# Performance work log

Measured on AMD Instinct MI355X. Metric: run time of the kernel, lower is better.

## Reference

```python
import jax, jax.numpy as jnp
import numpy as np

B, S, D, H = 2, 2048, 2048, 16
HD = D // H
ALIBI_BIAS_MAX = 8
NEG_INF = -1e9  # used only via float('-inf') literal below


def build_attn_mask(n_heads, seq_len, alibi_bias_max=8, dtype=jnp.float32):
    # causal mask: -inf strictly above diagonal
    causal = jnp.triu(jnp.full((seq_len, seq_len), -jnp.inf, dtype=dtype), k=1)
    # full alibi bias: -|i-j| scaled per head by 1/2**(m_h)
    rel = jnp.arange(1 - seq_len, 1, dtype=dtype)  # [S]
    bias = rel[None, :] - rel[:, None]             # [S,S]
    bias = -jnp.abs(bias)
    m = jnp.arange(1, n_heads + 1, dtype=dtype) * (alibi_bias_max / n_heads)
    slopes = 1.0 / (2.0 ** m)                      # [H]
    a_bias = bias[None, :, :] * slopes[:, None, None]  # [H,S,S]
    return causal[None, :, :] + a_bias


def setup_inputs() -> dict:
    key = jax.random.key(0)
    ks = jax.random.split(key, 6)
    x = jax.random.normal(ks[0], (B, S, D), dtype=jnp.float32)
    key_padding_mask = jnp.ones((B, S), dtype=bool)  # True = keep (module inverts before torch)
    attn_mask = build_attn_mask(H, S, ALIBI_BIAS_MAX)
    scale = 1.0 / np.sqrt(D)
    in_proj_w = jax.random.normal(ks[1], (3 * D, D), dtype=jnp.float32) * scale
    in_proj_b = jax.random.normal(ks[2], (3 * D,), dtype=jnp.float32) * 0.01
    out_w = jax.random.normal(ks[3], (D, D), dtype=jnp.float32) * scale
    out_b = jax.random.normal(ks[4], (D,), dtype=jnp.float32) * 0.01
    return {"x": x, "key_padding_mask": key_padding_mask, "attn_mask": attn_mask,
            "in_proj_w": in_proj_w, "in_proj_b": in_proj_b,
            "out_w": out_w, "out_b": out_b}


def reference(x, key_padding_mask, attn_mask, in_proj_w, in_proj_b, out_w, out_b):
    # fused QKV projection (torch MultiheadAttention in_proj)
    qkv = jnp.einsum('bsd,ed->bse', x, in_proj_w) + in_proj_b  # [B,S,3D]
    q, k, v = jnp.split(qkv, 3, axis=-1)
    # [B,H,S,hd]
    q = q.reshape(B, S, H, HD).transpose(0, 2, 1, 3)
    k = k.reshape(B, S, H, HD).transpose(0, 2, 1, 3)
    v = v.reshape(B, S, H, HD).transpose(0, 2, 1, 3)
    scores = jnp.einsum('bhqd,bhkd->bhqk', q, k) / jnp.sqrt(jnp.float32(HD))
    scores = scores + attn_mask[None]  # causal + alibi, [1,H,S,S]
    # key_padding_mask True = keep; masked keys -> -inf
    scores = jnp.where(key_padding_mask[:, None, None, :], scores, -jnp.inf)
    attn = jax.nn.softmax(scores, axis=-1)  # [B,H,S,S]
    ctx = jnp.einsum('bhqk,bhkd->bhqd', attn, v)
    ctx = ctx.transpose(0, 2, 1, 3).reshape(B, S, D)
    out = jnp.einsum('bsd,ed->bse', ctx, out_w) + out_b
    # need_weights=True, average_attn_weights default True -> mean over heads
    avg_attn = attn.mean(axis=1)  # [B,S,S]
    return out, avg_attn
```

## Files before the change

kernel.cpp:

```cpp
#include <hip/hip_runtime.h>
#include <math.h>

#define BB 2
#define SS 2048
#define DD 2048
#define HH 16
#define HDIM 128
#define QKVP 6144
#define NEG_INIT  -1.0e30f
#define NEG_CLAMP -3.0e4f

typedef __attribute__((ext_vector_type(8))) short s8v;
typedef __attribute__((ext_vector_type(4))) float f4v;

__device__ __forceinline__ short f2bf(float f) {
  unsigned u = __float_as_uint(f);
  unsigned r = (u + 0x7FFFu + ((u >> 16) & 1u)) >> 16;
  return (short)(unsigned short)r;
}

__global__ void conv_bf16(const float* __restrict__ src, short* __restrict__ dst,
                          int n8) {
  int t = blockIdx.x * blockDim.x + threadIdx.x;
  if (t >= n8) return;
  const float* s = src + (size_t)t * 8;
  s8v o;
#pragma unroll
  for (int i = 0; i < 8; i++) o[i] = f2bf(s[i]);
  ((s8v*)dst)[t] = o;
}

template <typename TOUT>
__global__ __launch_bounds__(256) void gemm_bt_bias(
    const short* __restrict__ A, const short* __restrict__ Bm,
    const float* __restrict__ bias, TOUT* __restrict__ C,
    int M, int N, int K)
{
  __shared__ short As[128 * 72];
  __shared__ short Bs[128 * 72];
  const int tid = threadIdx.x;
  const int lane = tid & 63, wid = tid >> 6;
  const int wm = wid >> 1, wn = wid & 1;
  const int ln = lane & 15, quad = lane >> 4;
  const int m0 = blockIdx.y * 128, n0 = blockIdx.x * 128;

  f4v acc[4][4];
#pragma unroll
  for (int i = 0; i < 4; i++)
#pragma unroll
    for (int j = 0; j < 4; j++) acc[i][j] = {0.f, 0.f, 0.f, 0.f};

  const int row = tid >> 1;
  const int ch  = (tid & 1) * 32;

  const s8v* ag = (const s8v*)(A + (size_t)(m0 + row) * K + ch);
  const s8v* bg = (const s8v*)(Bm + (size_t)(n0 + row) * K + ch);
  s8v a0 = ag[0], a1 = ag[1], a2 = ag[2], a3 = ag[3];
  s8v b0 = bg[0], b1 = bg[1], b2 = bg[2], b3 = bg[3];

  for (int kt = 0; kt < K; kt += 64) {
    __syncthreads();
    *(s8v*)&As[row * 72 + ch +  0] = a0;
    *(s8v*)&As[row * 72 + ch +  8] = a1;
    *(s8v*)&As[row * 72 + ch + 16] = a2;
    *(s8v*)&As[row * 72 + ch + 24] = a3;
    *(s8v*)&Bs[row * 72 + ch +  0] = b0;
    *(s8v*)&Bs[row * 72 + ch +  8] = b1;
    *(s8v*)&Bs[row * 72 + ch + 16] = b2;
    *(s8v*)&Bs[row * 72 + ch + 24] = b3;
    if (kt + 64 < K) {
      const s8v* an = (const s8v*)(A + (size_t)(m0 + row) * K + kt + 64 + ch);
      const s8v* bn = (const s8v*)(Bm + (size_t)(n0 + row) * K + kt + 64 + ch);
      a0 = an[0]; a1 = an[1]; a2 = an[2]; a3 = an[3];
      b0 = bn[0]; b1 = bn[1]; b2 = bn[2]; b3 = bn[3];
    }
    __syncthreads();
#pragma unroll
    for (int kc = 0; kc < 2; kc++) {
      s8v af[4], bfr[4];
#pragma unroll
      for (int i = 0; i < 4; i++)
        af[i] = *(const s8v*)&As[(wm * 64 + i * 16 + ln) * 72 + kc * 32 + quad * 8];
#pragma unroll
      for (int j = 0; j < 4; j++)
        bfr[j] = *(const s8v*)&Bs[(wn * 64 + j * 16 + ln) * 72 + kc * 32 + quad * 8];
#pragma unroll
      for (int i = 0; i < 4; i++)
#pragma unroll
        for (int j = 0; j < 4; j++)
          acc[i][j] = __builtin_amdgcn_mfma_f32_16x16x32_bf16(af[i], bfr[j], acc[i][j], 0, 0, 0);
    }
  }
#pragma unroll
  for (int j = 0; j < 4; j++) {
    int col = n0 + wn * 64 + j * 16 + ln;
    float bv = bias[col];
#pragma unroll
    for (int i = 0; i < 4; i++) {
      int rbase = m0 + wm * 64 + i * 16 + quad * 4;
#pragma unroll
      for (int r = 0; r < 4; r++) {
        float val = acc[i][j][r] + bv;
        if constexpr (sizeof(TOUT) == 4)
          C[(size_t)(rbase + r) * N + col] = val;
        else
          C[(size_t)(rbase + r) * N + col] = f2bf(val);
      }
    }
  }
}

__global__ __launch_bounds__(256) void transpose_v(const short* __restrict__ qkv,
                                                   short* __restrict__ vT) {
  __shared__ short tile[64 * 72];
  const int bh = blockIdx.z;
  const int b = bh >> 4;
  const int hsel = bh & 15;
  const int s0 = blockIdx.x * 64;
  const int hd0 = blockIdx.y * 64;
  const int t = threadIdx.x;
  const int r = t >> 3, c8 = t & 7;
#pragma unroll
  for (int half = 0; half < 2; half++) {
    int rr = r + half * 32;
    s8v v = *(const s8v*)&qkv[(size_t)(b * SS + s0 + rr) * QKVP + 4096 + hsel * HDIM + hd0 + c8 * 8];
    *(s8v*)&tile[rr * 72 + c8 * 8] = v;
  }
  __syncthreads();
#pragma unroll
  for (int half = 0; half < 2; half++) {
    int rr = r + half * 32;
    s8v o;
#pragma unroll
    for (int j = 0; j < 8; j++) o[j] = tile[(c8 * 8 + j) * 72 + rr];
    *(s8v*)&vT[((size_t)bh * HDIM + hd0 + rr) * SS + s0 + c8 * 8] = o;
  }
}

__global__ __launch_bounds__(512, 4) void flash_fwd(
    const short* __restrict__ qkv, const short* __restrict__ vT,
    float* __restrict__ lse, short* __restrict__ ctx)
{
  __shared__ short Ks[64 * 136];
  __shared__ short Vs[128 * 72];
  __shared__ short plds[8][16 * 72];

  const int g = blockIdx.x;
  const int b = g >> 8;
  const int h = (g >> 4) & 15;
  const int qh = g & 15;
  const int qt = b ? qh : 15 - qh;

  const int bh = b * HH + h;
  const int tid = threadIdx.x, lane = tid & 63, wid = tid >> 6;
  const int ln = lane & 15, quad = lane >> 4;
  const int q0 = qt * 128 + wid * 16;

  const short* qb = qkv + (size_t)b * SS * QKVP + h * HDIM;
  const short* kb = qb + 2048;
  const short* vb = vT + (size_t)bh * HDIM * SS;

  const int krow = tid >> 3, kc0 = (tid & 7) * 8;
  const int vrow = tid >> 2, vc0 = (tid & 3) * 8;
  const short* kgp = kb + (size_t)krow * QKVP + kc0;
  const short* vgp = vb + (size_t)vrow * SS + vc0;
  short* kls = &Ks[krow * 136 + kc0];
  short* vls = &Vs[vrow * 72 + vc0];

  const float slope = exp2f(-0.5f * (float)(h + 1));
  const float scale = 0.08838834764831845f;

  s8v aq[4];
#pragma unroll
  for (int kc = 0; kc < 4; kc++)
    aq[kc] = *(const s8v*)&qb[(size_t)(q0 + ln) * QKVP + kc * 32 + quad * 8];

  s8v k0r = ((const s8v*)kgp)[0], k1r = *(const s8v*)(kgp + 64);
  s8v v0r = ((const s8v*)vgp)[0], v1r = *(const s8v*)(vgp + 32);

  f4v o[8];
#pragma unroll
  for (int d = 0; d < 8; d++) o[d] = {0.f, 0.f, 0.f, 0.f};
  float mrow[4], lrow[4];
#pragma unroll
  for (int r = 0; r < 4; r++) { mrow[r] = NEG_INIT; lrow[r] = 0.0f; }

  const int nkt = 2 * qt + 2;
  for (int kt = 0; kt < nkt; kt++) {
    __syncthreads();
    *(s8v*)kls = k0r;  *(s8v*)(kls + 64) = k1r;
    *(s8v*)vls = v0r;  *(s8v*)(vls + 32) = v1r;
    if (kt < nkt - 1) {
      const short* kn = kgp + (size_t)(kt + 1) * 64 * QKVP;
      const short* vn = vgp + (kt + 1) * 64;
      k0r = ((const s8v*)kn)[0]; k1r = *(const s8v*)(kn + 64);
      v0r = ((const s8v*)vn)[0]; v1r = *(const s8v*)(vn + 32);
    }
    __syncthreads();

    if (kt * 64 > q0 + 15) continue;

    f4v sacc[4];
#pragma unroll
    for (int ks = 0; ks < 4; ks++) {
      f4v z = {0.f, 0.f, 0.f, 0.f};
#pragma unroll
      for (int kc = 0; kc < 4; kc++) {
        s8v bk = *(const s8v*)&Ks[(ks * 16 + ln) * 136 + kc * 32 + quad * 8];
        z = __builtin_amdgcn_mfma_f32_16x16x32_bf16(aq[kc], bk, z, 0, 0, 0);
      }
      sacc[ks] = z;
    }
    float sv[4][4];
#pragma unroll
    for (int ks = 0; ks < 4; ks++)
#pragma unroll
      for (int r = 0; r < 4; r++) {
        int i = q0 + quad * 4 + r;
        int j = kt * 64 + ks * 16 + ln;
        int di = i - j;
        sv[ks][r] = (di >= 0) ? fmaf(sacc[ks][r], scale, -(float)di * slope)
                              : NEG_CLAMP;
      }
    float mnew[4], al[4];
#pragma unroll
    for (int r = 0; r < 4; r++) {
      float mx = fmaxf(fmaxf(sv[0][r], sv[1][r]), fmaxf(sv[2][r], sv[3][r]));
#pragma unroll
      for (int off = 1; off < 16; off <<= 1)
        mx = fmaxf(mx, __shfl_xor(mx, off, 64));
      mnew[r] = fmaxf(mrow[r], mx);
      al[r] = __expf(mrow[r] - mnew[r]);
      mrow[r] = mnew[r];
    }
    float ps[4] = {0.f, 0.f, 0.f, 0.f};
    short pb[4][4];
#pragma unroll
    for (int ks = 0; ks < 4; ks++)
#pragma unroll
      for (int r = 0; r < 4; r++) {
        float p = __expf(sv[ks][r] - mnew[r]);
        ps[r] += p;
        pb[ks][r] = f2bf(p);
      }
#pragma unroll
    for (int r = 0; r < 4; r++) {
      float s = ps[r];
#pragma unroll
      for (int off = 1; off < 16; off <<= 1) s += __shfl_xor(s, off, 64);
      lrow[r] = lrow[r] * al[r] + s;
    }
#pragma unroll
    for (int d = 0; d < 8; d++)
#pragma unroll
      for (int r = 0; r < 4; r++) o[d][r] *= al[r];
#pragma unroll
    for (int ks = 0; ks < 4; ks++)
#pragma unroll
      for (int r = 0; r < 4; r++)
        plds[wid][(quad * 4 + r) * 72 + ks * 16 + ln] = pb[ks][r];
#pragma unroll
    for (int kc2 = 0; kc2 < 2; kc2++) {
      s8v ap = *(const s8v*)&plds[wid][ln * 72 + kc2 * 32 + quad * 8];
#pragma unroll
      for (int d = 0; d < 8; d++) {
        s8v bv = *(const s8v*)&Vs[(d * 16 + ln) * 72 + kc2 * 32 + quad * 8];
        o[d] = __builtin_amdgcn_mfma_f32_16x16x32_bf16(ap, bv, o[d], 0, 0, 0);
      }
    }
  }
  float inv[4];
#pragma unroll
  for (int r = 0; r < 4; r++) inv[r] = 1.0f / lrow[r];
#pragma unroll
  for (int d = 0; d < 8; d++)
#pragma unroll
    for (int r = 0; r < 4; r++) {
      int qrow = q0 + quad * 4 + r;
      ctx[((size_t)(b * SS + qrow)) * DD + h * HDIM + d * 16 + ln] = f2bf(o[d][r] * inv[r]);
    }
#pragma unroll
  for (int r = 0; r < 4; r++)
    if (ln == r)
      lse[(size_t)bh * SS + q0 + quad * 4 + r] = mrow[r] + __logf(lrow[r]);
}

__global__ __launch_bounds__(512, 4) void avg_attn_kernel(
    const short* __restrict__ qkv, const float* __restrict__ lse,
    float* __restrict__ avg)
{
  __shared__ short Ks[64 * 136];
  const int ktile = blockIdx.x, qtile = blockIdx.y, b = blockIdx.z;
  const int tid = threadIdx.x, lane = tid & 63, wid = tid >> 6;
  const int ln = lane & 15, quad = lane >> 4;
  const int q0 = qtile * 128 + wid * 16;
  const int k0 = ktile * 64;
  float acc[4][4];
#pragma unroll
  for (int ks = 0; ks < 4; ks++)
#pragma unroll
    for (int r = 0; r < 4; r++) acc[ks][r] = 0.0f;

  if (ktile <= 2 * qtile + 1) {
    const float scale = 0.08838834764831845f;
    const int krow = tid >> 3, kc0 = (tid & 7) * 8;
    const short* kg0 = qkv + (size_t)(b * SS + k0 + krow) * QKVP + 2048 + kc0;
    short* kls = &Ks[krow * 136 + kc0];
    s8v k0r = ((const s8v*)kg0)[0], k1r = *(const s8v*)(kg0 + 64);
    const bool wactive = (k0 <= q0 + 15);
    for (int hh = 0; hh < HH; hh++) {
      __syncthreads();
      *(s8v*)kls = k0r;  *(s8v*)(kls + 64) = k1r;
      if (hh < HH - 1) {
        const short* kn = kg0 + (hh + 1) * HDIM;
        k0r = ((const s8v*)kn)[0]; k1r = *(const s8v*)(kn + 64);
      }
      __syncthreads();
      if (wactive) {
        const int bh = b * HH + hh;
        const float slope = exp2f(-0.5f * (float)(hh + 1));
        const short* qb = qkv + (size_t)b * SS * QKVP + hh * HDIM;
        s8v aq[4];
#pragma unroll
        for (int kc = 0; kc < 4; kc++)
          aq[kc] = *(const s8v*)&qb[(size_t)(q0 + ln) * QKVP + kc * 32 + quad * 8];
        float lsev[4];
#pragma unroll
        for (int r = 0; r < 4; r++) lsev[r] = lse[(size_t)bh * SS + q0 + quad * 4 + r];
#pragma unroll
        for (int ks = 0; ks < 4; ks++) {
          f4v z = {0.f, 0.f, 0.f, 0.f};
#pragma unroll
          for (int kc = 0; kc < 4; kc++) {
            s8v bk = *(const s8v*)&Ks[(ks * 16 + ln) * 136 + kc * 32 + quad * 8];
            z = __builtin_amdgcn_mfma_f32_16x16x32_bf16(aq[kc], bk, z, 0, 0, 0);
          }
#pragma unroll
          for (int r = 0; r < 4; r++) {
            int i = q0 + quad * 4 + r;
            int j = k0 + ks * 16 + ln;
            int di = i - j;
            float svv = (di >= 0) ? fmaf(z[r], scale, -(float)di * slope) : NEG_CLAMP;
            acc[ks][r] += __expf(svv - lsev[r]);
          }
        }
      }
    }
  }
  const float inv16 = 1.0f / 16.0f;
#pragma unroll
  for (int ks = 0; ks < 4; ks++)
#pragma unroll
    for (int r = 0; r < 4; r++)
      avg[((size_t)b * SS + q0 + quad * 4 + r) * SS + k0 + ks * 16 + ln] =
          acc[ks][r] * inv16;
}

extern "C" void kernel_launch(void* const* d_in, const int* in_sizes, int n_in,
                              void* d_out, int out_size, void* d_ws, size_t ws_size,
                              hipStream_t stream)
{
  const float *x = nullptr, *w_in = nullptr, *b_in = nullptr,
              *w_out = nullptr, *b_out = nullptr;
  for (int idx = 0; idx < n_in; idx++) {
    switch (in_sizes[idx]) {
      case 8388608:  x     = (const float*)d_in[idx]; break;
      case 12582912: w_in  = (const float*)d_in[idx]; break;
      case 6144:     b_in  = (const float*)d_in[idx]; break;
      case 4194304:  w_out = (const float*)d_in[idx]; break;
      case 2048:     b_out = (const float*)d_in[idx]; break;
      default: break;
    }
  }

  char* ws = (char*)d_ws;
  short* qkv = (short*)(ws);
  short* xb  = (short*)(ws + 50331648);
  short* vT  = (short*)(ws + 50331648);
  short* wib = (short*)(ws + 67108864);
  short* ctx = (short*)(ws + 67108864);
  float* lse = (float*)(ws + 83886080);
  short* wob = (short*)(ws + 92274688);

  float* outp = (float*)d_out;
  float* avgp = outp + (size_t)BB * SS * DD;

  conv_bf16<<<4096, 256, 0, stream>>>(x, xb, 1048576);
  conv_bf16<<<6144, 256, 0, stream>>>(w_in, wib, 1572864);
  conv_bf16<<<2048, 256, 0, stream>>>(w_out, wob, 524288);

  gemm_bt_bias<short><<<dim3(QKVP / 128, (BB * SS) / 128), 256, 0, stream>>>(
      xb, wib, b_in, qkv, BB * SS, QKVP, DD);
  transpose_v<<<dim3(32, 2, 32), 256, 0, stream>>>(qkv, vT);
  flash_fwd<<<dim3(512, 1, 1), 512, 0, stream>>>(qkv, vT, lse, ctx);
  avg_attn_kernel<<<dim3(32, 16, 2), 512, 0, stream>>>(qkv, lse, avgp);
  gemm_bt_bias<float><<<dim3(DD / 128, (BB * SS) / 128), 256, 0, stream>>>(
      ctx, wob, b_out, outp, BB * SS, DD, DD);
}
```

Baseline: 719.9 us.

## Use direct global-to-LDS loads in GEMM, widen avg-attn key tiles, skip masked subtiles

The GEMM now stages A/B tiles with global_load_lds (direct-to-LDS) instead of a register double buffer, and drops the LDS row padding. This removes VGPR staging and store instructions but also loses the prefetch overlap and padding, so LDS bank conflicts are possible. The avg-attention kernel processes 128-key tiles per block, halving redundant Q/LSE reloads, and skips fully masked 16-key subtiles per wave. Flash forward also skips the QK MFMAs for masked 16-key subtiles on diagonal tiles.

```diff
diff --git a/kernel.cpp b/kernel.cpp
--- a/kernel.cpp
+++ b/kernel.cpp
@@ -13,6 +13,13 @@
 typedef __attribute__((ext_vector_type(8))) short s8v;
 typedef __attribute__((ext_vector_type(4))) float f4v;
 
+typedef const unsigned __attribute__((address_space(1)))* gas_ptr;
+typedef unsigned __attribute__((address_space(3)))* las_ptr;
+
+__device__ __forceinline__ void gld16(const short* g, short* l) {
+  __builtin_amdgcn_global_load_lds((gas_ptr)g, (las_ptr)l, 16, 0, 0);
+}
+
 __device__ __forceinline__ short f2bf(float f) {
   unsigned u = __float_as_uint(f);
   unsigned r = (u + 0x7FFFu + ((u >> 16) & 1u)) >> 16;
@@ -36,8 +43,8 @@
     const float* __restrict__ bias, TOUT* __restrict__ C,
     int M, int N, int K)
 {
-  __shared__ short As[128 * 72];
-  __shared__ short Bs[128 * 72];
+  __shared__ short As[128 * 64];
+  __shared__ short Bs[128 * 64];
   const int tid = threadIdx.x;
   const int lane = tid & 63, wid = tid >> 6;
   const int wm = wid >> 1, wn = wid & 1;
@@ -50,29 +57,17 @@
 #pragma unroll
     for (int j = 0; j < 4; j++) acc[i][j] = {0.f, 0.f, 0.f, 0.f};
 
-  const int row = tid >> 1;
-  const int ch  = (tid & 1) * 32;
-
-  const s8v* ag = (const s8v*)(A + (size_t)(m0 + row) * K + ch);
-  const s8v* bg = (const s8v*)(Bm + (size_t)(n0 + row) * K + ch);
-  s8v a0 = ag[0], a1 = ag[1], a2 = ag[2], a3 = ag[3];
-  s8v b0 = bg[0], b1 = bg[1], b2 = bg[2], b3 = bg[3];
+  const int srow = (lane >> 3);
+  const int scol = (lane & 7) * 8;
 
   for (int kt = 0; kt < K; kt += 64) {
+    const short* a_g = A  + (size_t)(m0 + wid * 32 + srow) * K + kt + scol;
+    const short* b_g = Bm + (size_t)(n0 + wid * 32 + srow) * K + kt + scol;
     __syncthreads();
-    *(s8v*)&As[row * 72 + ch +  0] = a0;
-    *(s8v*)&As[row * 72 + ch +  8] = a1;
-    *(s8v*)&As[row * 72 + ch + 16] = a2;
-    *(s8v*)&As[row * 72 + ch + 24] = a3;
-    *(s8v*)&Bs[row * 72 + ch +  0] = b0;
-    *(s8v*)&Bs[row * 72 + ch +  8] = b1;
-    *(s8v*)&Bs[row * 72 + ch + 16] = b2;
-    *(s8v*)&Bs[row * 72 + ch + 24] = b3;
-    if (kt + 64 < K) {
-      const s8v* an = (const s8v*)(A + (size_t)(m0 + row) * K + kt + 64 + ch);
-      const s8v* bn = (const s8v*)(Bm + (size_t)(n0 + row) * K + kt + 64 + ch);
-      a0 = an[0]; a1 = an[1]; a2 = an[2]; a3 = an[3];
-      b0 = bn[0]; b1 = bn[1]; b2 = bn[2]; b3 = bn[3];
+#pragma unroll
+    for (int i = 0; i < 4; i++) {
+      gld16(a_g + (size_t)i * 8 * K, &As[(wid * 32 + i * 8) * 64]);
+      gld16(b_g + (size_t)i * 8 * K, &Bs[(wid * 32 + i * 8) * 64]);
     }
     __syncthreads();
 #pragma unroll
@@ -80,10 +75,10 @@
       s8v af[4], bfr[4];
 #pragma unroll
       for (int i = 0; i < 4; i++)
-        af[i] = *(const s8v*)&As[(wm * 64 + i * 16 + ln) * 72 + kc * 32 + quad * 8];
+        af[i] = *(const s8v*)&As[(wm * 64 + i * 16 + ln) * 64 + kc * 32 + quad * 8];
 #pragma unroll
       for (int j = 0; j < 4; j++)
-        bfr[j] = *(const s8v*)&Bs[(wn * 64 + j * 16 + ln) * 72 + kc * 32 + quad * 8];
+        bfr[j] = *(const s8v*)&Bs[(wn * 64 + j * 16 + ln) * 64 + kc * 32 + quad * 8];
 #pragma unroll
       for (int i = 0; i < 4; i++)
 #pragma unroll
@@ -204,10 +199,12 @@
 #pragma unroll
     for (int ks = 0; ks < 4; ks++) {
       f4v z = {0.f, 0.f, 0.f, 0.f};
-#pragma unroll
-      for (int kc = 0; kc < 4; kc++) {
-        s8v bk = *(const s8v*)&Ks[(ks * 16 + ln) * 136 + kc * 32 + quad * 8];
-        z = __builtin_amdgcn_mfma_f32_16x16x32_bf16(aq[kc], bk, z, 0, 0, 0);
+      if (kt * 64 + ks * 16 <= q0 + 15) {
+#pragma unroll
+        for (int kc = 0; kc < 4; kc++) {
+          s8v bk = *(const s8v*)&Ks[(ks * 16 + ln) * 136 + kc * 32 + quad * 8];
+          z = __builtin_amdgcn_mfma_f32_16x16x32_bf16(aq[kc], bk, z, 0, 0, 0);
+        }
       }
       sacc[ks] = z;
     }
@@ -289,67 +286,69 @@
     const short* __restrict__ qkv, const float* __restrict__ lse,
     float* __restrict__ avg)
 {
-  __shared__ short Ks[64 * 136];
+  __shared__ short Ks[128 * 136];
   const int ktile = blockIdx.x, qtile = blockIdx.y, b = blockIdx.z;
   const int tid = threadIdx.x, lane = tid & 63, wid = tid >> 6;
   const int ln = lane & 15, quad = lane >> 4;
   const int q0 = qtile * 128 + wid * 16;
-  const int k0 = ktile * 64;
-  float acc[4][4];
-#pragma unroll
-  for (int ks = 0; ks < 4; ks++)
+  const int k0 = ktile * 128;
+  float acc[8][4];
+#pragma unroll
+  for (int ks = 0; ks < 8; ks++)
 #pragma unroll
     for (int r = 0; r < 4; r++) acc[ks][r] = 0.0f;
 
-  if (ktile <= 2 * qtile + 1) {
+  if (ktile <= qtile) {
     const float scale = 0.08838834764831845f;
-    const int krow = tid >> 3, kc0 = (tid & 7) * 8;
-    const short* kg0 = qkv + (size_t)(b * SS + k0 + krow) * QKVP + 2048 + kc0;
-    short* kls = &Ks[krow * 136 + kc0];
-    s8v k0r = ((const s8v*)kg0)[0], k1r = *(const s8v*)(kg0 + 64);
-    const bool wactive = (k0 <= q0 + 15);
+    const int krow = tid >> 2, kch = (tid & 3) * 8;
+    const short* kg0 = qkv + (size_t)(b * SS + k0 + krow) * QKVP + 2048 + kch;
+    short* kls = &Ks[krow * 136 + kch];
+    s8v kreg[4];
+#pragma unroll
+    for (int j = 0; j < 4; j++) kreg[j] = *(const s8v*)(kg0 + j * 32);
     for (int hh = 0; hh < HH; hh++) {
       __syncthreads();
-      *(s8v*)kls = k0r;  *(s8v*)(kls + 64) = k1r;
+#pragma unroll
+      for (int j = 0; j < 4; j++) *(s8v*)(kls + j * 32) = kreg[j];
       if (hh < HH - 1) {
         const short* kn = kg0 + (hh + 1) * HDIM;
-        k0r = ((const s8v*)kn)[0]; k1r = *(const s8v*)(kn + 64);
+#pragma unroll
+        for (int j = 0; j < 4; j++) kreg[j] = *(const s8v*)(kn + j * 32);
       }
       __syncthreads();
-      if (wactive) {
-        const int bh = b * HH + hh;
-        const float slope = exp2f(-0.5f * (float)(hh + 1));
-        const short* qb = qkv + (size_t)b * SS * QKVP + hh * HDIM;
-        s8v aq[4];
-#pragma unroll
-        for (int kc = 0; kc < 4; kc++)
-          aq[kc] = *(const s8v*)&qb[(size_t)(q0 + ln) * QKVP + kc * 32 + quad * 8];
-        float lsev[4];
-#pragma unroll
-        for (int r = 0; r < 4; r++) lsev[r] = lse[(size_t)bh * SS + q0 + quad * 4 + r];
-#pragma unroll
-        for (int ks = 0; ks < 4; ks++) {
-          f4v z = {0.f, 0.f, 0.f, 0.f};
-#pragma unroll
-          for (int kc = 0; kc < 4; kc++) {
-            s8v bk = *(const s8v*)&Ks[(ks * 16 + ln) * 136 + kc * 32 + quad * 8];
-            z = __builtin_amdgcn_mfma_f32_16x16x32_bf16(aq[kc], bk, z, 0, 0, 0);
-          }
-#pragma unroll
-          for (int r = 0; r < 4; r++) {
-            int i = q0 + quad * 4 + r;
-            int j = k0 + ks * 16 + ln;
-            int di = i - j;
-            float svv = (di >= 0) ? fmaf(z[r], scale, -(float)di * slope) : NEG_CLAMP;
-            acc[ks][r] += __expf(svv - lsev[r]);
-          }
+      const int bh = b * HH + hh;
+      const float slope = exp2f(-0.5f * (float)(hh + 1));
+      const short* qb = qkv + (size_t)b * SS * QKVP + hh * HDIM;
+      s8v aq[4];
+#pragma unroll
+      for (int kc = 0; kc < 4; kc++)
+        aq[kc] = *(const s8v*)&qb[(size_t)(q0 + ln) * QKVP + kc * 32 + quad * 8];
+      float lsev[4];
+#pragma unroll
+      for (int r = 0; r < 4; r++) lsev[r] = lse[(size_t)bh * SS + q0 + quad * 4 + r];
+#pragma unroll
+      for (int ks = 0; ks < 8; ks++) {
+        if (k0 + ks * 16 > q0 + 15) continue;
+        f4v z = {0.f, 0.f, 0.f, 0.f};
+#pragma unroll
+        for (int kc = 0; kc < 4; kc++) {
+          s8v bk = *(const s8v*)&Ks[(ks * 16 + ln) * 136 + kc * 32 + quad * 8];
+          z = __builtin_amdgcn_mfma_f32_16x16x32_bf16(aq[kc], bk, z, 0, 0, 0);
         }
+#pragma unroll
+        for (int r = 0; r < 4; r++) {
+          int i = q0 + quad * 4 + r;
+          int j = k0 + ks * 16 + ln;
+          int di = i - j;
+          float svv = (di >= 0) ? fmaf(z[r], scale, -(float)di * slope) : NEG_CLAMP;
+          acc[ks][r] += __expf(svv - lsev[r]);
+        }
       }
     }
   }
   const float inv16 = 1.0f / 16.0f;
 #pragma unroll
-  for (int ks = 0; ks < 4; ks++)
+  for (int ks = 0; ks < 8; ks++)
 #pragma unroll
     for (int r = 0; r < 4; r++)
       avg[((size_t)b * SS + q0 + quad * 4 + r) * SS + k0 + ks * 16 + ln] =
@@ -393,7 +392,7 @@
       xb, wib, b_in, qkv, BB * SS, QKVP, DD);
   transpose_v<<<dim3(32, 2, 32), 256, 0, stream>>>(qkv, vT);
   flash_fwd<<<dim3(512, 1, 1), 512, 0, stream>>>(qkv, vT, lse, ctx);
-  avg_attn_kernel<<<dim3(32, 16, 2), 512, 0, stream>>>(qkv, lse, avgp);
+  avg_attn_kernel<<<dim3(16, 16, 2), 512, 0, stream>>>(qkv, lse, avgp);
   gemm_bt_bias<float><<<dim3(DD / 128, (BB * SS) / 128), 256, 0, stream>>>(
       ctx, wob, b_out, outp, BB * SS, DD, DD);
 }
```

Result: no change. 722.1 us (+0.3%).
